# Kernel tuning notes

Hardware: AMD Instinct MI355X
Metric: run time of the kernel (lower is better)

Reference implementation:

```python
import jax, jax.numpy as jnp
import numpy as np

N_NODES = 100000
N_EDGES = 1600000
IN_C, HID_C, OUT_C = 128, 128, 64


def setup_inputs() -> dict:
    key = jax.random.key(0)
    ks = jax.random.split(key, 8)
    x = jax.random.normal(ks[0], (N_NODES, IN_C), dtype=jnp.float32)
    edge_index = jax.random.randint(ks[1], (2, N_EDGES), 0, N_NODES, dtype=jnp.int64)
    # SAGEConv params: lin_l (aggregated neighbors, with bias), lin_r (root, no bias)
    s1 = 1.0 / np.sqrt(IN_C)
    s2 = 1.0 / np.sqrt(HID_C)
    W1_l = jax.random.uniform(ks[2], (IN_C, HID_C), jnp.float32, -s1, s1)
    b1_l = jnp.zeros((HID_C,), jnp.float32)
    W1_r = jax.random.uniform(ks[3], (IN_C, HID_C), jnp.float32, -s1, s1)
    W2_l = jax.random.uniform(ks[4], (HID_C, OUT_C), jnp.float32, -s2, s2)
    b2_l = jnp.zeros((OUT_C,), jnp.float32)
    W2_r = jax.random.uniform(ks[5], (HID_C, OUT_C), jnp.float32, -s2, s2)
    return {"x": x, "edge_index": edge_index, "W1_l": W1_l, "b1_l": b1_l,
            "W1_r": W1_r, "W2_l": W2_l, "b2_l": b2_l, "W2_r": W2_r}


def _sage_conv(x, src, dst, W_l, b_l, W_r):
    # gather source features, scatter-max reduce onto destinations
    msg = x[src]                                             # [E, C]
    aggr = jax.ops.segment_max(msg, dst, num_segments=N_NODES)
    aggr = jnp.where(jnp.isfinite(aggr), aggr, 0.0)          # isolated nodes -> 0 (PyG behavior)
    return aggr @ W_l + b_l + x @ W_r


def reference(x, edge_index, W1_l, b1_l, W1_r, W2_l, b2_l, W2_r):
    src, dst = edge_index[0], edge_index[1]
    h = _sage_conv(x, src, dst, W1_l, b1_l, W1_r)
    h = jax.nn.relu(h)
    # dropout is identity in eval mode
    out = _sage_conv(h, src, dst, W2_l, b2_l, W2_r)
    return out
```

## Files before the change

kernel.cpp:

```cpp
#include <hip/hip_runtime.h>
#include <cstdint>

#define NNODES 100000
#define NEDGES 1600000
#define NBKT   196
#define CAP    9216
#define BIN_CHUNK 4096
#define KP 136
#define GBIN ((NEDGES + BIN_CHUNK - 1) / BIN_CHUNK)
#define GCVT (NNODES * 128 / 8 / 256)

typedef __attribute__((ext_vector_type(8))) __bf16 bf16x8;
typedef __attribute__((ext_vector_type(4))) float f32x4;
typedef short v2s __attribute__((ext_vector_type(2)));

__device__ __forceinline__ unsigned short f2bf_rne(float f) {
    unsigned int u = __float_as_uint(f);
    u += 0x7fffu + ((u >> 16) & 1u);
    return (unsigned short)(u >> 16);
}
__device__ __forceinline__ unsigned encdec(unsigned u) {
    return u ^ (((u & 0x80008000u) >> 15) * 0x7FFFu);
}
__device__ __forceinline__ unsigned pkmax(unsigned a, unsigned b) {
    v2s r = __builtin_elementwise_max(__builtin_bit_cast(v2s, a), __builtin_bit_cast(v2s, b));
    return __builtin_bit_cast(unsigned, r);
}

__global__ __launch_bounds__(256) void prep1_kernel(
        const float* __restrict__ W1l, const float* __restrict__ W1r,
        const float* __restrict__ W2l, const float* __restrict__ W2r,
        unsigned short* __restrict__ T1l, unsigned short* __restrict__ T1r,
        unsigned short* __restrict__ T2l, unsigned short* __restrict__ T2r,
        int* __restrict__ bucketFill) {
    if (blockIdx.x == 64) { bucketFill[threadIdx.x] = 0; return; }
    int i = blockIdx.x * 256 + threadIdx.x;
    int k = i >> 7, n = i & 127;
    T1l[n * KP + k] = f2bf_rne(W1l[i]);
    T1r[n * KP + k] = f2bf_rne(W1r[i]);
    if (i < 128 * 64) {
        int k2 = i >> 6, n2 = i & 63;
        T2l[n2 * KP + k2] = f2bf_rne(W2l[i]);
        T2r[n2 * KP + k2] = f2bf_rne(W2r[i]);
    }
}

__global__ __launch_bounds__(256) void prep2_kernel(
        const int* __restrict__ src, const int* __restrict__ dst,
        unsigned int* __restrict__ binArr, int* __restrict__ bucketFill,
        const float4* __restrict__ xin, uint4* __restrict__ xeout, int nE) {
    if (blockIdx.x >= GBIN) {
        int i = (blockIdx.x - GBIN) * 256 + threadIdx.x;
        float4 v0 = xin[(size_t)2 * i], v1 = xin[(size_t)2 * i + 1];
        uint4 o;
        o.x = encdec((unsigned)f2bf_rne(v0.x) | ((unsigned)f2bf_rne(v0.y) << 16));
        o.y = encdec((unsigned)f2bf_rne(v0.z) | ((unsigned)f2bf_rne(v0.w) << 16));
        o.z = encdec((unsigned)f2bf_rne(v1.x) | ((unsigned)f2bf_rne(v1.y) << 16));
        o.w = encdec((unsigned)f2bf_rne(v1.z) | ((unsigned)f2bf_rne(v1.w) << 16));
        xeout[i] = o;
        return;
    }
    __shared__ unsigned int stage[BIN_CHUNK];
    __shared__ unsigned char bof[BIN_CHUNK];
    __shared__ int cnt[256], cstart[256], cfill[256], gbase[256];
    const int tid = threadIdx.x;
    const int blockStart = blockIdx.x * BIN_CHUNK;
    const int chunkN = min(BIN_CHUNK, nE - blockStart);
    cnt[tid] = 0;
    __syncthreads();
    int myd[16], mys[16];
#pragma unroll
    for (int i = 0; i < 16; ++i) {
        int idx = i * 256 + tid;
        if (idx < chunkN) {
            myd[i] = dst[blockStart + idx];
            mys[i] = src[blockStart + idx];
            atomicAdd(&cnt[myd[i] >> 9], 1);
        }
    }
    __syncthreads();
    int v = cnt[tid];
    for (int off = 1; off < 256; off <<= 1) {
        int add = (tid >= off) ? cnt[tid - off] : 0;
        __syncthreads();
        cnt[tid] += add;
        __syncthreads();
    }
    cstart[tid] = cnt[tid] - v;
    cfill[tid] = cnt[tid] - v;
    if (tid < NBKT && v > 0) gbase[tid] = atomicAdd(&bucketFill[tid], v);
    __syncthreads();
#pragma unroll
    for (int i = 0; i < 16; ++i) {
        int idx = i * 256 + tid;
        if (idx < chunkN) {
            int b = myd[i] >> 9;
            int p = atomicAdd(&cfill[b], 1);
            stage[p] = ((unsigned)(myd[i] & 511) << 17) | (unsigned)mys[i];
            bof[p] = (unsigned char)b;
        }
    }
    __syncthreads();
#pragma unroll
    for (int i = 0; i < 16; ++i) {
        int idx = i * 256 + tid;
        if (idx < chunkN) {
            int b = bof[idx];
            int slot = gbase[b] + (idx - cstart[b]);
            if (slot < CAP) binArr[(size_t)b * CAP + slot] = stage[idx];
        }
    }
}

__global__ __launch_bounds__(512) void build_csr_kernel(
        const unsigned int* __restrict__ binArr, const int* __restrict__ bucketFill,
        unsigned int* __restrict__ sortedSrc,
        int* __restrict__ rowBeg, int* __restrict__ rowEnd) {
    __shared__ unsigned int stage[CAP];
    __shared__ int ncnt[512], nstart[512];
    const int b = blockIdx.x;
    const int t = threadIdx.x;
    const int cnt_b = min(bucketFill[b], CAP);
    ncnt[t] = 0;
    __syncthreads();
    for (int i = t; i < cnt_b; i += 512) {
        unsigned int e = binArr[(size_t)b * CAP + i];
        stage[i] = e;
        atomicAdd(&ncnt[e >> 17], 1);
    }
    __syncthreads();
    int v = ncnt[t];
    for (int off = 1; off < 512; off <<= 1) {
        int add = (t >= off) ? ncnt[t - off] : 0;
        __syncthreads();
        ncnt[t] += add;
        __syncthreads();
    }
    int start = ncnt[t] - v;
    nstart[t] = start;
    int n = (b << 9) + t;
    if (n < NNODES) {
        rowBeg[n] = b * CAP + start;
        rowEnd[n] = b * CAP + start + v;
    }
    __syncthreads();
    for (int i = t; i < cnt_b; i += 512) {
        unsigned int e = stage[i];
        int p = atomicAdd(&nstart[e >> 17], 1);
        sortedSrc[(size_t)b * CAP + p] = e & 0x1FFFFu;
    }
}

template<int BN, bool RELU, bool ENCOUT, typename OutT>
__global__ __launch_bounds__(256, 4) void sage_fused(
        const uint4* __restrict__ xe4,
        const int* __restrict__ rowBeg,
        const int* __restrict__ rowEnd,
        const unsigned int* __restrict__ sortedSrc,
        const unsigned short* __restrict__ Wtl,
        const unsigned short* __restrict__ Wtr,
        const float* __restrict__ bias,
        OutT* __restrict__ C,
        int M) {
    constexpr int NT = BN / 16;
    __shared__ __align__(16) unsigned short As[64 * KP];
    __shared__ __align__(16) unsigned short Bs[BN * 68];

    const int tid = threadIdx.x;
    const int w = tid >> 6;
    const int lane = tid & 63;
    const int grp = lane >> 4;
    const int c16 = lane & 15;
    const int mrow = lane & 15;
    const int quad = lane >> 4;
    const int base0 = blockIdx.x * 64;

    int bl = 0, el = 0;
    {
        int nn = base0 + w * 16 + (lane & 15);
        if (nn < M) { bl = rowBeg[nn]; el = rowEnd[nn]; }
    }
    int nbeg = __shfl(bl, 0), nend = __shfl(el, 0);
    int nid = (nend > nbeg) ? (int)sortedSrc[min(nbeg + lane, nend - 1)] : 0;
    for (int i = 0; i < 16; ++i) {
        const int beg = nbeg, end = nend;
        const int myid = nid;
        if (i < 15) {
            nbeg = __shfl(bl, i + 1);
            nend = __shfl(el, i + 1);
            nid = (nend > nbeg) ? (int)sortedSrc[min(nbeg + lane, nend - 1)] : 0;
        }
        const int r = w * 16 + i;
        if (end <= beg) {
            if (lane < 16) {
                uint4 z; z.x = z.y = z.z = z.w = 0u;
                ((uint4*)As)[r * 17 + c16] = z;
            }
            continue;
        }
        unsigned a0 = 0x80008000u, a1 = 0x80008000u, a2 = 0x80008000u, a3 = 0x80008000u;
        {
            const int m = min(end - beg, 64);
            for (int j = 0; j < m; j += 16) {
                int s0 = __shfl(myid, j + grp);
                int s1 = __shfl(myid, j + 4 + grp);
                int s2 = __shfl(myid, j + 8 + grp);
                int s3 = __shfl(myid, j + 12 + grp);
                uint4 p0 = xe4[(size_t)s0 * 16 + c16];
                uint4 p1 = xe4[(size_t)s1 * 16 + c16];
                uint4 p2 = xe4[(size_t)s2 * 16 + c16];
                uint4 p3 = xe4[(size_t)s3 * 16 + c16];
                a0 = pkmax(a0, pkmax(pkmax(p0.x, p1.x), pkmax(p2.x, p3.x)));
                a1 = pkmax(a1, pkmax(pkmax(p0.y, p1.y), pkmax(p2.y, p3.y)));
                a2 = pkmax(a2, pkmax(pkmax(p0.z, p1.z), pkmax(p2.z, p3.z)));
                a3 = pkmax(a3, pkmax(pkmax(p0.w, p1.w), pkmax(p2.w, p3.w)));
            }
        }
        for (int bs = beg + 64; bs < end; bs += 64) {
            int bid = (int)sortedSrc[min(bs + lane, end - 1)];
            const int m = min(end - bs, 64);
            for (int j = 0; j < m; j += 16) {
                int s0 = __shfl(bid, j + grp);
                int s1 = __shfl(bid, j + 4 + grp);
                int s2 = __shfl(bid, j + 8 + grp);
                int s3 = __shfl(bid, j + 12 + grp);
                uint4 p0 = xe4[(size_t)s0 * 16 + c16];
                uint4 p1 = xe4[(size_t)s1 * 16 + c16];
                uint4 p2 = xe4[(size_t)s2 * 16 + c16];
                uint4 p3 = xe4[(size_t)s3 * 16 + c16];
                a0 = pkmax(a0, pkmax(pkmax(p0.x, p1.x), pkmax(p2.x, p3.x)));
                a1 = pkmax(a1, pkmax(pkmax(p0.y, p1.y), pkmax(p2.y, p3.y)));
                a2 = pkmax(a2, pkmax(pkmax(p0.z, p1.z), pkmax(p2.z, p3.z)));
                a3 = pkmax(a3, pkmax(pkmax(p0.w, p1.w), pkmax(p2.w, p3.w)));
            }
        }
        a0 = pkmax(a0, (unsigned)__shfl_xor((int)a0, 16));
        a1 = pkmax(a1, (unsigned)__shfl_xor((int)a1, 16));
        a2 = pkmax(a2, (unsigned)__shfl_xor((int)a2, 16));
        a3 = pkmax(a3, (unsigned)__shfl_xor((int)a3, 16));
        a0 = pkmax(a0, (unsigned)__shfl_xor((int)a0, 32));
        a1 = pkmax(a1, (unsigned)__shfl_xor((int)a1, 32));
        a2 = pkmax(a2, (unsigned)__shfl_xor((int)a2, 32));
        a3 = pkmax(a3, (unsigned)__shfl_xor((int)a3, 32));
        if (lane < 16) {
            uint4 o;
            o.x = encdec(a0); o.y = encdec(a1); o.z = encdec(a2); o.w = encdec(a3);
            ((uint4*)As)[r * 17 + c16] = o;
        }
    }

    f32x4 acc[NT];
#pragma unroll
    for (int nt = 0; nt < NT; ++nt) acc[nt] = (f32x4){0.f, 0.f, 0.f, 0.f};
    __syncthreads();

    for (int half = 0; half < 2; ++half) {
        if (half == 1) {
            __syncthreads();
            const uint2* xs = (const uint2*)xe4;
            for (int i2 = tid; i2 < 64 * 32; i2 += 256) {
                int r = i2 >> 5, c = i2 & 31;
                int gr = base0 + r;
                if (gr >= M) gr = 0;
                uint2 vv = xs[(size_t)gr * 32 + c];
                vv.x = encdec(vv.x); vv.y = encdec(vv.y);
                ((uint2*)As)[r * 34 + c] = vv;
            }
        }
        const unsigned short* Wt = half ? Wtr : Wtl;
        for (int ks = 0; ks < 2; ++ks) {
            __syncthreads();
            const uint2* wsrc = (const uint2*)Wt;
            for (int i2 = tid; i2 < BN * 16; i2 += 256) {
                int n = i2 >> 4, c = i2 & 15;
                ((uint2*)Bs)[n * 17 + c] = wsrc[n * 34 + ks * 16 + c];
            }
            __syncthreads();
#pragma unroll
            for (int kt2 = 0; kt2 < 2; ++kt2) {
                bf16x8 a = *(const bf16x8*)(As + (w * 16 + mrow) * KP +
                                            ks * 64 + kt2 * 32 + quad * 8);
#pragma unroll
                for (int nt = 0; nt < NT; ++nt) {
                    bf16x8 b = *(const bf16x8*)(Bs + (nt * 16 + mrow) * 68 +
                                                kt2 * 32 + quad * 8);
                    acc[nt] = __builtin_amdgcn_mfma_f32_16x16x32_bf16(a, b, acc[nt], 0, 0, 0);
                }
            }
        }
    }

    const int rowD = base0 + w * 16 + quad * 4;
#pragma unroll
    for (int nt = 0; nt < NT; ++nt) {
        int col = nt * 16 + mrow;
        float bv = bias[col];
#pragma unroll
        for (int r = 0; r < 4; ++r) {
            int grow = rowD + r;
            if (grow < M) {
                float v = acc[nt][r] + bv;
                if (RELU) v = fmaxf(v, 0.0f);
                if constexpr (ENCOUT) {
                    unsigned u = f2bf_rne(v);
                    u ^= ((u >> 15) & 1u) * 0x7FFFu;
                    C[(size_t)grow * BN + col] = (OutT)u;
                } else {
                    C[(size_t)grow * BN + col] = (OutT)v;
                }
            }
        }
    }
}

extern "C" void kernel_launch(void* const* d_in, const int* in_sizes, int n_in,
                              void* d_out, int out_size, void* d_ws, size_t ws_size,
                              hipStream_t stream) {
    const float* x   = (const float*)d_in[0];
    const int*   ei  = (const int*)d_in[1];
    const float* W1l = (const float*)d_in[2];
    const float* b1l = (const float*)d_in[3];
    const float* W1r = (const float*)d_in[4];
    const float* W2l = (const float*)d_in[5];
    const float* b2l = (const float*)d_in[6];
    const float* W2r = (const float*)d_in[7];
    float* out = (float*)d_out;

    const int* src = ei;
    const int* dst = ei + NEDGES;

    char* ws = (char*)d_ws;
    unsigned short* xe = (unsigned short*)ws; ws += (size_t)NNODES * 128 * 2;
    unsigned short* he = (unsigned short*)ws; ws += (size_t)NNODES * 128 * 2;
    unsigned int* binArr    = (unsigned int*)ws; ws += (size_t)NBKT * CAP * 4;
    unsigned int* sortedSrc = (unsigned int*)ws; ws += (size_t)NBKT * CAP * 4;
    int* rowBeg     = (int*)ws; ws += (size_t)NNODES * 4;
    int* rowEnd     = (int*)ws; ws += (size_t)NNODES * 4;
    int* bucketFill = (int*)ws; ws += 256 * 4;
    unsigned short* T1l = (unsigned short*)ws; ws += 128 * KP * 2;
    unsigned short* T1r = (unsigned short*)ws; ws += 128 * KP * 2;
    unsigned short* T2l = (unsigned short*)ws; ws += 64 * KP * 2;
    unsigned short* T2r = (unsigned short*)ws; ws += 64 * KP * 2;

    const int gGemm = (NNODES + 63) / 64;

    prep1_kernel<<<65, 256, 0, stream>>>(W1l, W1r, W2l, W2r, T1l, T1r, T2l, T2r, bucketFill);
    prep2_kernel<<<GBIN + GCVT, 256, 0, stream>>>(src, dst, binArr, bucketFill,
                                                  (const float4*)x, (uint4*)xe, NEDGES);
    build_csr_kernel<<<NBKT, 512, 0, stream>>>(binArr, bucketFill, sortedSrc, rowBeg, rowEnd);

    sage_fused<128, true, true, unsigned short><<<gGemm, 256, 0, stream>>>(
        (const uint4*)xe, rowBeg, rowEnd, sortedSrc, T1l, T1r, b1l, he, NNODES);
    sage_fused<64, false, false, float><<<gGemm, 256, 0, stream>>>(
        (const uint4*)he, rowBeg, rowEnd, sortedSrc, T2l, T2r, b2l, out, NNODES);
}
```

Baseline: 304.2 us.

## Pre-swizzle weights into MFMA fragment layout and read B directly from global

```diff
diff --git a/kernel.cpp b/kernel.cpp
--- a/kernel.cpp
+++ b/kernel.cpp
@@ -6,7 +6,6 @@
 #define NBKT   196
 #define CAP    9216
 #define BIN_CHUNK 4096
-#define KP 136
 #define GBIN ((NEDGES + BIN_CHUNK - 1) / BIN_CHUNK)
 #define GCVT (NNODES * 128 / 8 / 256)
 
@@ -30,18 +29,38 @@
 __global__ __launch_bounds__(256) void prep1_kernel(
         const float* __restrict__ W1l, const float* __restrict__ W1r,
         const float* __restrict__ W2l, const float* __restrict__ W2r,
-        unsigned short* __restrict__ T1l, unsigned short* __restrict__ T1r,
-        unsigned short* __restrict__ T2l, unsigned short* __restrict__ T2r,
+        uint4* __restrict__ Wf1, uint4* __restrict__ Wf2,
         int* __restrict__ bucketFill) {
-    if (blockIdx.x == 64) { bucketFill[threadIdx.x] = 0; return; }
-    int i = blockIdx.x * 256 + threadIdx.x;
-    int k = i >> 7, n = i & 127;
-    T1l[n * KP + k] = f2bf_rne(W1l[i]);
-    T1r[n * KP + k] = f2bf_rne(W1r[i]);
-    if (i < 128 * 64) {
-        int k2 = i >> 6, n2 = i & 63;
-        T2l[n2 * KP + k2] = f2bf_rne(W2l[i]);
-        T2r[n2 * KP + k2] = f2bf_rne(W2r[i]);
+    if (blockIdx.x == 24) { bucketFill[threadIdx.x] = 0; return; }
+    int t = blockIdx.x * 256 + threadIdx.x;
+    unsigned short s[8];
+    if (t < 4096) {
+        int h = t >> 11, kt = (t >> 9) & 3, nt = (t >> 6) & 7, lane = t & 63;
+        const float* W = h ? W1r : W1l;
+        int k0 = kt * 32 + (lane >> 4) * 8;
+        int col = nt * 16 + (lane & 15);
+#pragma unroll
+        for (int j = 0; j < 8; ++j) s[j] = f2bf_rne(W[(k0 + j) * 128 + col]);
+        uint4 o;
+        o.x = (unsigned)s[0] | ((unsigned)s[1] << 16);
+        o.y = (unsigned)s[2] | ((unsigned)s[3] << 16);
+        o.z = (unsigned)s[4] | ((unsigned)s[5] << 16);
+        o.w = (unsigned)s[6] | ((unsigned)s[7] << 16);
+        Wf1[t] = o;
+    } else {
+        int u = t - 4096;
+        int h = u >> 10, kt = (u >> 8) & 3, nt = (u >> 6) & 3, lane = u & 63;
+        const float* W = h ? W2r : W2l;
+        int k0 = kt * 32 + (lane >> 4) * 8;
+        int col = nt * 16 + (lane & 15);
+#pragma unroll
+        for (int j = 0; j < 8; ++j) s[j] = f2bf_rne(W[(k0 + j) * 64 + col]);
+        uint4 o;
+        o.x = (unsigned)s[0] | ((unsigned)s[1] << 16);
+        o.y = (unsigned)s[2] | ((unsigned)s[3] << 16);
+        o.z = (unsigned)s[4] | ((unsigned)s[5] << 16);
+        o.w = (unsigned)s[6] | ((unsigned)s[7] << 16);
+        Wf2[u] = o;
     }
 }
 
@@ -152,32 +171,28 @@
 }
 
 template<int BN, bool RELU, bool ENCOUT, typename OutT>
-__global__ __launch_bounds__(256, 4) void sage_fused(
+__global__ __launch_bounds__(256, 6) void sage_fused(
         const uint4* __restrict__ xe4,
         const int* __restrict__ rowBeg,
         const int* __restrict__ rowEnd,
         const unsigned int* __restrict__ sortedSrc,
-        const unsigned short* __restrict__ Wtl,
-        const unsigned short* __restrict__ Wtr,
+        const uint4* __restrict__ Wf,
         const float* __restrict__ bias,
         OutT* __restrict__ C,
         int M) {
     constexpr int NT = BN / 16;
-    __shared__ __align__(16) unsigned short As[64 * KP];
-    __shared__ __align__(16) unsigned short Bs[BN * 68];
+    __shared__ __align__(16) unsigned short As[64 * 136];
 
     const int tid = threadIdx.x;
     const int w = tid >> 6;
     const int lane = tid & 63;
     const int grp = lane >> 4;
     const int c16 = lane & 15;
-    const int mrow = lane & 15;
-    const int quad = lane >> 4;
     const int base0 = blockIdx.x * 64;
 
     int bl = 0, el = 0;
     {
-        int nn = base0 + w * 16 + (lane & 15);
+        int nn = base0 + w * 16 + c16;
         if (nn < M) { bl = rowBeg[nn]; el = rowEnd[nn]; }
     }
     int nbeg = __shfl(bl, 0), nend = __shfl(el, 0);
@@ -252,48 +267,28 @@
     f32x4 acc[NT];
 #pragma unroll
     for (int nt = 0; nt < NT; ++nt) acc[nt] = (f32x4){0.f, 0.f, 0.f, 0.f};
-    __syncthreads();
-
-    for (int half = 0; half < 2; ++half) {
-        if (half == 1) {
-            __syncthreads();
-            const uint2* xs = (const uint2*)xe4;
-            for (int i2 = tid; i2 < 64 * 32; i2 += 256) {
-                int r = i2 >> 5, c = i2 & 31;
-                int gr = base0 + r;
-                if (gr >= M) gr = 0;
-                uint2 vv = xs[(size_t)gr * 32 + c];
-                vv.x = encdec(vv.x); vv.y = encdec(vv.y);
-                ((uint2*)As)[r * 34 + c] = vv;
-            }
-        }
-        const unsigned short* Wt = half ? Wtr : Wtl;
-        for (int ks = 0; ks < 2; ++ks) {
-            __syncthreads();
-            const uint2* wsrc = (const uint2*)Wt;
-            for (int i2 = tid; i2 < BN * 16; i2 += 256) {
-                int n = i2 >> 4, c = i2 & 15;
-                ((uint2*)Bs)[n * 17 + c] = wsrc[n * 34 + ks * 16 + c];
-            }
-            __syncthreads();
-#pragma unroll
-            for (int kt2 = 0; kt2 < 2; ++kt2) {
-                bf16x8 a = *(const bf16x8*)(As + (w * 16 + mrow) * KP +
-                                            ks * 64 + kt2 * 32 + quad * 8);
-#pragma unroll
-                for (int nt = 0; nt < NT; ++nt) {
-                    bf16x8 b = *(const bf16x8*)(Bs + (nt * 16 + mrow) * 68 +
-                                                kt2 * 32 + quad * 8);
-                    acc[nt] = __builtin_amdgcn_mfma_f32_16x16x32_bf16(a, b, acc[nt], 0, 0, 0);
-                }
-            }
-        }
-    }
-
-    const int rowD = base0 + w * 16 + quad * 4;
+
+    const int rowR = base0 + w * 16 + c16;
+    const int rowRc = (rowR < M) ? rowR : 0;
+#pragma unroll
+    for (int kt = 0; kt < 4; ++kt) {
+        bf16x8 aa = *(const bf16x8*)(As + (w * 16 + c16) * 136 + kt * 32 + grp * 8);
+        uint4 tr = xe4[(size_t)rowRc * 16 + kt * 4 + grp];
+        tr.x = encdec(tr.x); tr.y = encdec(tr.y); tr.z = encdec(tr.z); tr.w = encdec(tr.w);
+        bf16x8 ar = __builtin_bit_cast(bf16x8, tr);
+#pragma unroll
+        for (int nt = 0; nt < NT; ++nt) {
+            bf16x8 b0 = __builtin_bit_cast(bf16x8, Wf[(kt * NT + nt) * 64 + lane]);
+            acc[nt] = __builtin_amdgcn_mfma_f32_16x16x32_bf16(aa, b0, acc[nt], 0, 0, 0);
+            bf16x8 b1 = __builtin_bit_cast(bf16x8, Wf[((4 + kt) * NT + nt) * 64 + lane]);
+            acc[nt] = __builtin_amdgcn_mfma_f32_16x16x32_bf16(ar, b1, acc[nt], 0, 0, 0);
+        }
+    }
+
+    const int rowD = base0 + w * 16 + grp * 4;
 #pragma unroll
     for (int nt = 0; nt < NT; ++nt) {
-        int col = nt * 16 + mrow;
+        int col = nt * 16 + c16;
         float bv = bias[col];
 #pragma unroll
         for (int r = 0; r < 4; ++r) {
@@ -337,20 +332,18 @@
     int* rowBeg     = (int*)ws; ws += (size_t)NNODES * 4;
     int* rowEnd     = (int*)ws; ws += (size_t)NNODES * 4;
     int* bucketFill = (int*)ws; ws += 256 * 4;
-    unsigned short* T1l = (unsigned short*)ws; ws += 128 * KP * 2;
-    unsigned short* T1r = (unsigned short*)ws; ws += 128 * KP * 2;
-    unsigned short* T2l = (unsigned short*)ws; ws += 64 * KP * 2;
-    unsigned short* T2r = (unsigned short*)ws; ws += 64 * KP * 2;
+    uint4* Wf1 = (uint4*)ws; ws += 4096 * 16;
+    uint4* Wf2 = (uint4*)ws; ws += 2048 * 16;
 
     const int gGemm = (NNODES + 63) / 64;
 
-    prep1_kernel<<<65, 256, 0, stream>>>(W1l, W1r, W2l, W2r, T1l, T1r, T2l, T2r, bucketFill);
+    prep1_kernel<<<25, 256, 0, stream>>>(W1l, W1r, W2l, W2r, Wf1, Wf2, bucketFill);
     prep2_kernel<<<GBIN + GCVT, 256, 0, stream>>>(src, dst, binArr, bucketFill,
                                                   (const float4*)x, (uint4*)xe, NEDGES);
     build_csr_kernel<<<NBKT, 512, 0, stream>>>(binArr, bucketFill, sortedSrc, rowBeg, rowEnd);
 
     sage_fused<128, true, true, unsigned short><<<gGemm, 256, 0, stream>>>(
-        (const uint4*)xe, rowBeg, rowEnd, sortedSrc, T1l, T1r, b1l, he, NNODES);
+        (const uint4*)xe, rowBeg, rowEnd, sortedSrc, Wf1, b1l, he, NNODES);
     sage_fused<64, false, false, float><<<gGemm, 256, 0, stream>>>(
-        (const uint4*)he, rowBeg, rowEnd, sortedSrc, T2l, T2r, b2l, out, NNODES);
-}
+        (const uint4*)he, rowBeg, rowEnd, sortedSrc, Wf2, b2l, out, NNODES);
+}
```

After: 297.9 us. -2.1%, faster.
